# Performance work log

Measured on AMD Instinct MI355X. Metric: run time of the kernel, lower is better.

## Reference

```python
import jax, jax.numpy as jnp
import numpy as np

D_MODEL = 1024
H = 16
D_K = D_MODEL // H


def setup_inputs() -> dict:
    key = jax.random.key(0)
    ks = jax.random.split(key, 10)
    B, S = 2, 2048
    s = 1.0 / np.sqrt(D_MODEL)
    x = jax.random.normal(ks[0], (B, S, D_MODEL), dtype=jnp.float32)
    mask = jax.random.randint(ks[1], (B, 1, S, S), 0, 2, dtype=jnp.int32)
    w_q = jax.random.normal(ks[2], (D_MODEL, D_MODEL), dtype=jnp.float32) * s
    b_q = jnp.zeros((D_MODEL,), dtype=jnp.float32)
    w_k = jax.random.normal(ks[3], (D_MODEL, D_MODEL), dtype=jnp.float32) * s
    b_k = jnp.zeros((D_MODEL,), dtype=jnp.float32)
    w_v = jax.random.normal(ks[4], (D_MODEL, D_MODEL), dtype=jnp.float32) * s
    b_v = jnp.zeros((D_MODEL,), dtype=jnp.float32)
    w_o = jax.random.normal(ks[5], (D_MODEL, D_MODEL), dtype=jnp.float32) * s
    b_o = jnp.zeros((D_MODEL,), dtype=jnp.float32)
    return {"x": x, "mask": mask, "w_q": w_q, "b_q": b_q, "w_k": w_k,
            "b_k": b_k, "w_v": w_v, "b_v": b_v, "w_o": w_o, "b_o": b_o}


def reference(x, mask, w_q, b_q, w_k, b_k, w_v, b_v, w_o, b_o):
    B, S, _ = x.shape
    # projections; weights stored as (in, out) equivalents of torch Linear
    q = (x @ w_q + b_q).reshape(B, S, H, D_K).transpose(0, 2, 1, 3)  # bhsd
    k = (x @ w_k + b_k).reshape(B, S, H, D_K).transpose(0, 2, 1, 3)
    v = (x @ w_v + b_v).reshape(B, S, H, D_K).transpose(0, 2, 1, 3)
    scores = jnp.einsum('bhqd,bhkd->bhqk', q, k) / jnp.sqrt(jnp.float32(D_K))
    scores = jnp.where(mask == 0, jnp.float32(-1e9), scores)
    attn = jax.nn.softmax(scores, axis=-1)  # dropout omitted (eval mode)
    out = jnp.einsum('bhqk,bhkd->bhqd', attn, v)
    out = out.transpose(0, 2, 1, 3).reshape(B, S, D_MODEL)
    return out @ w_o + b_o
```

## Files before the change

### kernel.cpp

```cpp
#include <hip/hip_runtime.h>
#include <hip/hip_bf16.h>
#include <stdint.h>

#define D_MODEL 1024
#define NH 16
#define DK 64
#define SEQ 2048
#define BATCH 2
#define NTOK (BATCH * SEQ)

typedef __bf16 bf16;
typedef float f32x4 __attribute__((ext_vector_type(4)));
typedef __bf16 bf16x8 __attribute__((ext_vector_type(8)));
typedef __bf16 bf16x4 __attribute__((ext_vector_type(4)));
typedef __bf16 bf16x2 __attribute__((ext_vector_type(2)));

#define QSCALE 0.18033687932432668f

__device__ __forceinline__ void gload_lds16(const void* g, void* l) {
  __builtin_amdgcn_global_load_lds(
      (const __attribute__((address_space(1))) void*)g,
      (__attribute__((address_space(3))) void*)l, 16, 0, 0);
}

__global__ void prep_kernel(const float* __restrict__ x, bf16* __restrict__ xb,
                            const float* __restrict__ wq, const float* __restrict__ wk,
                            const float* __restrict__ wv, const float* __restrict__ wo,
                            bf16* __restrict__ wt,
                            const int* __restrict__ mask, unsigned long long* __restrict__ bits) {
  __shared__ float tile[32][33];
  const int bx = blockIdx.x;
  const int tid = threadIdx.x;
  if (bx < 4096) {
    int i = bx * 256 + tid;
    float4 v = reinterpret_cast<const float4*>(x)[i];
    bf16x4 o;
    o[0] = (bf16)v.x; o[1] = (bf16)v.y; o[2] = (bf16)v.z; o[3] = (bf16)v.w;
    reinterpret_cast<bf16x4*>(xb)[i] = o;
  } else if (bx < 8192) {
    int blk = bx - 4096;
    const int jt = blk & 127;
    const int kt = blk >> 7;
    const int tx = tid & 31, ty = tid >> 5;
    const int j0 = jt * 32;
    const int sel = j0 >> 10;
    const float* w = (sel == 0) ? wq : (sel == 1) ? wk : (sel == 2) ? wv : wo;
    const int jj0 = j0 & 1023;
#pragma unroll
    for (int i = 0; i < 4; ++i)
      tile[ty + i * 8][tx] = w[(size_t)(kt * 32 + ty + i * 8) * 1024 + jj0 + tx];
    __syncthreads();
#pragma unroll
    for (int i = 0; i < 4; ++i)
      wt[(size_t)(j0 + ty + i * 8) * 1024 + kt * 32 + tx] = (bf16)tile[tx][ty + i * 8];
  } else {
    int gt = (bx - 8192) * 256 + tid;
    int wid = gt >> 6;
    int l = gt & 63;
    int m = mask[(size_t)wid * 64 + l];
    unsigned long long b = __ballot(m != 0);
    if (l == 0) bits[wid] = b;
  }
}

__global__ __launch_bounds__(256) void gemm_qkv(
    const bf16* __restrict__ A, const bf16* __restrict__ Bt,
    const float* __restrict__ b0, const float* __restrict__ b1, const float* __restrict__ b2,
    bf16* __restrict__ out_q, bf16* __restrict__ out_k, bf16* __restrict__ out_vt) {
  __shared__ __align__(16) bf16 As[2][128 * 32];
  __shared__ __align__(16) bf16 Bs[2][128 * 32];
  const int tid = threadIdx.x;
  const int w = tid >> 6, l = tid & 63;
  const int wr = w >> 1, wc = w & 1;
  int lin = blockIdx.x + 24 * blockIdx.y;
  int nl = (lin & 7) * 96 + (lin >> 3);
  const int m0 = (nl / 24) * 128, n0 = (nl % 24) * 128;
  f32x4 acc[4][4] = {};
  const int lrow = l >> 2;
  const int lc8 = (l & 3) * 8;

  auto STAGE = [&](int buf, int k0) {
    char* AsB = (char*)As[buf];
    char* BsB = (char*)Bs[buf];
#pragma unroll
    for (int is = 0; is < 2; ++is) {
      int arow = m0 + is * 64 + w * 16 + lrow;
      gload_lds16(A + (size_t)arow * 1024 + k0 + lc8, AsB + is * 4096 + w * 1024);
      int brow = n0 + is * 64 + w * 16 + lrow;
      gload_lds16(Bt + (size_t)brow * 1024 + k0 + lc8, BsB + is * 4096 + w * 1024);
    }
  };

  STAGE(0, 0);
  for (int it = 0; it < 32; ++it) {
    const int cur = it & 1;
    if (it < 31) {
      STAGE(cur ^ 1, (it + 1) * 32);
      __builtin_amdgcn_sched_barrier(0);
      asm volatile("s_waitcnt vmcnt(4)" ::: "memory");
    } else {
      __builtin_amdgcn_sched_barrier(0);
      asm volatile("s_waitcnt vmcnt(0)" ::: "memory");
    }
    __builtin_amdgcn_s_barrier();
    __builtin_amdgcn_sched_barrier(0);
    const bf16* Asc = As[cur];
    const bf16* Bsc = Bs[cur];
    bf16x8 af[4], bfr[4];
#pragma unroll
    for (int m = 0; m < 4; ++m)
      af[m] = *reinterpret_cast<const bf16x8*>(Asc + (wr * 64 + m * 16 + (l & 15)) * 32 + (l >> 4) * 8);
#pragma unroll
    for (int n = 0; n < 4; ++n)
      bfr[n] = *reinterpret_cast<const bf16x8*>(Bsc + (wc * 64 + n * 16 + (l & 15)) * 32 + (l >> 4) * 8);
#pragma unroll
    for (int m = 0; m < 4; ++m)
#pragma unroll
      for (int n = 0; n < 4; ++n)
        acc[m][n] = __builtin_amdgcn_mfma_f32_16x16x32_bf16(af[m], bfr[n], acc[m][n], 0, 0, 0);
    __builtin_amdgcn_sched_barrier(0);
    __builtin_amdgcn_s_barrier();
  }

#pragma unroll
  for (int m = 0; m < 4; ++m) {
    int ib = m0 + wr * 64 + m * 16 + 4 * (l >> 4);
#pragma unroll
    for (int n = 0; n < 4; ++n) {
      int j = n0 + wc * 64 + n * 16 + (l & 15);
      int sel = j >> 10, jj = j & 1023;
      const float* bp = (sel == 0) ? b0 : (sel == 1) ? b1 : b2;
      float bias = bp[jj];
      if (sel == 0) {
#pragma unroll
        for (int r = 0; r < 4; ++r)
          out_q[(size_t)(ib + r) * 1024 + jj] = (bf16)((acc[m][n][r] + bias) * QSCALE);
      } else if (sel == 1) {
#pragma unroll
        for (int r = 0; r < 4; ++r)
          out_k[(size_t)(ib + r) * 1024 + jj] = (bf16)(acc[m][n][r] + bias);
      } else {
        int hh = jj >> 6, dd = jj & 63;
        int bb = ib >> 11, ss = ib & 2047;
        bf16x4 v;
#pragma unroll
        for (int r = 0; r < 4; ++r) v[r] = (bf16)(acc[m][n][r] + bias);
        *reinterpret_cast<bf16x4*>(out_vt + ((size_t)(bb * NH + hh) * DK + dd) * SEQ + ss) = v;
      }
    }
  }
}

__global__ __launch_bounds__(256) void gemm_out(
    const bf16* __restrict__ A, const bf16* __restrict__ Bt,
    const float* __restrict__ bias, float* __restrict__ out) {
  __shared__ __align__(16) bf16 As[2][128 * 32];
  __shared__ __align__(16) bf16 Bs[2][64 * 32];
  const int tid = threadIdx.x;
  const int w = tid >> 6, l = tid & 63;
  const int wr = w >> 1, wc = w & 1;
  int lin = blockIdx.x + 16 * blockIdx.y;
  int nl = (lin & 7) * 64 + (lin >> 3);
  const int m0 = (nl >> 4) * 128, n0 = (nl & 15) * 64;
  f32x4 acc[4][2] = {};
  const int lrow = l >> 2;
  const int lc8 = (l & 3) * 8;

  auto STAGE = [&](int buf, int k0) {
    char* AsB = (char*)As[buf];
    char* BsB = (char*)Bs[buf];
#pragma unroll
    for (int is = 0; is < 2; ++is) {
      int arow = m0 + is * 64 + w * 16 + lrow;
      gload_lds16(A + (size_t)arow * 1024 + k0 + lc8, AsB + is * 4096 + w * 1024);
    }
    gload_lds16(Bt + (size_t)(n0 + w * 16 + lrow) * 1024 + k0 + lc8, BsB + w * 1024);
  };

  STAGE(0, 0);
  for (int it = 0; it < 32; ++it) {
    const int cur = it & 1;
    if (it < 31) {
      STAGE(cur ^ 1, (it + 1) * 32);
      __builtin_amdgcn_sched_barrier(0);
      asm volatile("s_waitcnt vmcnt(3)" ::: "memory");
    } else {
      __builtin_amdgcn_sched_barrier(0);
      asm volatile("s_waitcnt vmcnt(0)" ::: "memory");
    }
    __builtin_amdgcn_s_barrier();
    __builtin_amdgcn_sched_barrier(0);
    const bf16* Asc = As[cur];
    const bf16* Bsc = Bs[cur];
    bf16x8 af[4], bfr[2];
#pragma unroll
    for (int m = 0; m < 4; ++m)
      af[m] = *reinterpret_cast<const bf16x8*>(Asc + (wr * 64 + m * 16 + (l & 15)) * 32 + (l >> 4) * 8);
#pragma unroll
    for (int n = 0; n < 2; ++n)
      bfr[n] = *reinterpret_cast<const bf16x8*>(Bsc + (wc * 32 + n * 16 + (l & 15)) * 32 + (l >> 4) * 8);
#pragma unroll
    for (int m = 0; m < 4; ++m)
#pragma unroll
      for (int n = 0; n < 2; ++n)
        acc[m][n] = __builtin_amdgcn_mfma_f32_16x16x32_bf16(af[m], bfr[n], acc[m][n], 0, 0, 0);
    __builtin_amdgcn_sched_barrier(0);
    __builtin_amdgcn_s_barrier();
  }

#pragma unroll
  for (int m = 0; m < 4; ++m) {
    int ib = m0 + wr * 64 + m * 16 + 4 * (l >> 4);
#pragma unroll
    for (int n = 0; n < 2; ++n) {
      int j = n0 + wc * 32 + n * 16 + (l & 15);
      float bv = bias[j];
#pragma unroll
      for (int r = 0; r < 4; ++r)
        out[(size_t)(ib + r) * 1024 + j] = acc[m][n][r] + bv;
    }
  }
}

__global__ __launch_bounds__(256, 4) void attn_kernel(
    const bf16* __restrict__ qb, const bf16* __restrict__ kb,
    const bf16* __restrict__ vt, const unsigned long long* __restrict__ mbits,
    bf16* __restrict__ ob) {
  __shared__ __align__(16) bf16 Kbuf[2][64 * 64];
  __shared__ __align__(16) bf16 Vbuf[2][64 * 64];
  __shared__ __align__(16) bf16 Ps[4][16 * 64];
  const int tid = threadIdx.x;
  const int w = tid >> 6, l = tid & 63;
  int lin = blockIdx.x + 32 * blockIdx.y + 512 * blockIdx.z;
  int nl = (lin & 7) * 128 + (lin >> 3);
  const int qt = nl & 31, h = (nl >> 5) & 15, b = nl >> 9;
  const int q0 = qt * 64;
  const int qrow = q0 + w * 16;
  const int tok0 = b * SEQ + qrow;
  const int a = l >> 4, c = l & 15;

  bf16x8 qf[2];
#pragma unroll
  for (int kk = 0; kk < 2; ++kk)
    qf[kk] = *reinterpret_cast<const bf16x8*>(
        qb + (size_t)(tok0 + c) * 1024 + h * 64 + kk * 32 + a * 8);

  float lsum = 0.f;
  f32x4 oacc[4] = {};

  const int swz = ((l & 7) ^ (l >> 3)) * 8;
  const bf16* ksrc = kb + (size_t)(b * SEQ) * 1024 + h * 64;
  const bf16* vsrc = vt + (size_t)(b * NH + h) * DK * SEQ;
  const unsigned long long* mrow = mbits + ((size_t)(b * SEQ + qrow + c) << 5);

  auto STAGE = [&](int buf, int kt) {
    char* KsB = (char*)Kbuf[buf];
    char* VsB = (char*)Vbuf[buf];
#pragma unroll
    for (int i = 0; i < 2; ++i) {
      int row = i * 32 + w * 8 + (l >> 3);
      gload_lds16(ksrc + (size_t)(kt * 64 + row) * 1024 + swz, KsB + i * 4096 + w * 1024);
      gload_lds16(vsrc + (size_t)row * SEQ + kt * 64 + swz, VsB + i * 4096 + w * 1024);
    }
  };

  STAGE(0, 0);
  for (int kt = 0; kt < 32; ++kt) {
    const int cur = kt & 1;
    unsigned long long mw = mrow[kt];
    __builtin_amdgcn_sched_barrier(0);
    if (kt < 31) {
      STAGE(cur ^ 1, kt + 1);
      __builtin_amdgcn_sched_barrier(0);
      asm volatile("s_waitcnt vmcnt(8)" ::: "memory");
    } else {
      __builtin_amdgcn_sched_barrier(0);
      asm volatile("s_waitcnt vmcnt(0)" ::: "memory");
    }
    __builtin_amdgcn_s_barrier();
    __builtin_amdgcn_sched_barrier(0);

    const bf16* Ks = Kbuf[cur];
    const bf16* Vs = Vbuf[cur];

    f32x4 sa[4] = {};
#pragma unroll
    for (int kk = 0; kk < 2; ++kk) {
      bf16x8 kf[4];
      int cc = kk * 4 + a;
#pragma unroll
      for (int n = 0; n < 4; ++n) {
        int rr = n * 16 + c;
        kf[n] = *reinterpret_cast<const bf16x8*>(Ks + rr * 64 + ((cc ^ (rr & 7)) << 3));
      }
#pragma unroll
      for (int n = 0; n < 4; ++n)
        sa[n] = __builtin_amdgcn_mfma_f32_16x16x32_bf16(kf[n], qf[kk], sa[n], 0, 0, 0);
    }

    unsigned long long base = mw >> (a * 4);
    float ps[4][4];
#pragma unroll
    for (int n = 0; n < 4; ++n)
#pragma unroll
      for (int r = 0; r < 4; ++r) {
        bool on = (base >> (16 * n + r)) & 1ull;
        float p = on ? __builtin_amdgcn_exp2f(sa[n][r]) : 0.f;
        ps[n][r] = p;
        lsum += p;
      }
#pragma unroll
    for (int n = 0; n < 4; ++n)
#pragma unroll
      for (int pp = 0; pp < 2; ++pp) {
        int chunk = (2 * n + (a >> 1)) ^ (c & 7);
        bf16x2 v2 = {(bf16)ps[n][2 * pp], (bf16)ps[n][2 * pp + 1]};
        *reinterpret_cast<bf16x2*>(Ps[w] + c * 64 + chunk * 8 + 4 * (a & 1) + 2 * pp) = v2;
      }

#pragma unroll
    for (int kk = 0; kk < 2; ++kk) {
      bf16x8 pa = *reinterpret_cast<const bf16x8*>(Ps[w] + c * 64 + (((a + 4 * kk) ^ (c & 7)) << 3));
      bf16x8 vf[4];
#pragma unroll
      for (int dn = 0; dn < 4; ++dn) {
        int rr = dn * 16 + c;
        vf[dn] = *reinterpret_cast<const bf16x8*>(Vs + rr * 64 + (((kk * 4 + a) ^ (rr & 7)) << 3));
      }
#pragma unroll
      for (int dn = 0; dn < 4; ++dn)
        oacc[dn] = __builtin_amdgcn_mfma_f32_16x16x32_bf16(pa, vf[dn], oacc[dn], 0, 0, 0);
    }
    __builtin_amdgcn_sched_barrier(0);
    __builtin_amdgcn_s_barrier();
  }

  float s = lsum;
  s += __shfl_xor(s, 16);
  s += __shfl_xor(s, 32);
#pragma unroll
  for (int r = 0; r < 4; ++r) {
    float sr = __shfl(s, 4 * a + r);
    float inv = 1.f / fmaxf(sr, 1e-35f);
    int tok = tok0 + 4 * a + r;
#pragma unroll
    for (int dn = 0; dn < 4; ++dn)
      ob[(size_t)tok * 1024 + h * 64 + dn * 16 + c] = (bf16)(oacc[dn][r] * inv);
  }
}

extern "C" void kernel_launch(void* const* d_in, const int* in_sizes, int n_in,
                              void* d_out, int out_size, void* d_ws, size_t ws_size,
                              hipStream_t stream) {
  const float* x = (const float*)d_in[0];
  const int* mask = (const int*)d_in[1];
  const float* wq = (const float*)d_in[2];
  const float* bq = (const float*)d_in[3];
  const float* wk = (const float*)d_in[4];
  const float* bk = (const float*)d_in[5];
  const float* wv = (const float*)d_in[6];
  const float* bv = (const float*)d_in[7];
  const float* wo = (const float*)d_in[8];
  const float* bo = (const float*)d_in[9];
  float* out = (float*)d_out;

  char* ws = (char*)d_ws;
  bf16* xb = (bf16*)(ws + (size_t)0);
  bf16* wt = (bf16*)(ws + ((size_t)8 << 20));
  bf16* qb = (bf16*)(ws + ((size_t)16 << 20));
  bf16* kb = (bf16*)(ws + ((size_t)24 << 20));
  bf16* vtb = (bf16*)(ws + ((size_t)32 << 20));
  bf16* ob = (bf16*)(ws + ((size_t)40 << 20));
  unsigned long long* mbits = (unsigned long long*)(ws + ((size_t)48 << 20));

  prep_kernel<<<40960, 256, 0, stream>>>(x, xb, wq, wk, wv, wo, wt, mask, mbits);
  gemm_qkv<<<dim3(24, 32), 256, 0, stream>>>(xb, wt, bq, bk, bv, qb, kb, vtb);
  attn_kernel<<<dim3(32, NH, BATCH), 256, 0, stream>>>(qb, kb, vtb, mbits, ob);
  gemm_out<<<dim3(16, 32), 256, 0, stream>>>(ob, wt + (size_t)3072 * 1024, bo, out);
}
```

Measured before the change: 234.4 us.

## Use single-buffered BK=64 swizzled GEMM tiles, XCD-aware block mapping, tweak attention waits

Both projection GEMMs drop the double-buffered BK=32 pipeline and use a single LDS buffer with BK=64 and an XOR-swizzled layout, with plain __syncthreads between the load and compute phases. Block-to-tile mapping is reworked so each XCD owns a contiguous band of N columns, which is meant to improve L2 reuse of the weights. In attention, the vmcnt wait count changes from 8 to 5 and the P-tile stores widen from bf16x2 to bf16x4. Giving up double buffering exposes global load latency in exchange for fewer barriers and conflict-free LDS reads. The vmcnt(5) value looks inconsistent with 4 outstanding loads per stage and may over-wait or under-wait.

Result: no change. 238.5 us (+1.8%).

```diff
diff --git a/kernel.cpp b/kernel.cpp
--- a/kernel.cpp
+++ b/kernel.cpp
@@ -13,7 +13,6 @@
 typedef float f32x4 __attribute__((ext_vector_type(4)));
 typedef __bf16 bf16x8 __attribute__((ext_vector_type(8)));
 typedef __bf16 bf16x4 __attribute__((ext_vector_type(4)));
-typedef __bf16 bf16x2 __attribute__((ext_vector_type(2)));
 
 #define QSCALE 0.18033687932432668f
 
@@ -67,59 +66,45 @@
     const bf16* __restrict__ A, const bf16* __restrict__ Bt,
     const float* __restrict__ b0, const float* __restrict__ b1, const float* __restrict__ b2,
     bf16* __restrict__ out_q, bf16* __restrict__ out_k, bf16* __restrict__ out_vt) {
-  __shared__ __align__(16) bf16 As[2][128 * 32];
-  __shared__ __align__(16) bf16 Bs[2][128 * 32];
+  __shared__ __align__(16) bf16 As[128 * 64];
+  __shared__ __align__(16) bf16 Bs[128 * 64];
   const int tid = threadIdx.x;
   const int w = tid >> 6, l = tid & 63;
   const int wr = w >> 1, wc = w & 1;
   int lin = blockIdx.x + 24 * blockIdx.y;
-  int nl = (lin & 7) * 96 + (lin >> 3);
-  const int m0 = (nl / 24) * 128, n0 = (nl % 24) * 128;
+  int xcd = lin & 7, idx = lin >> 3;
+  const int n0 = (xcd * 3 + idx % 3) * 128;
+  const int m0 = (idx / 3) * 128;
   f32x4 acc[4][4] = {};
-  const int lrow = l >> 2;
-  const int lc8 = (l & 3) * 8;
-
-  auto STAGE = [&](int buf, int k0) {
-    char* AsB = (char*)As[buf];
-    char* BsB = (char*)Bs[buf];
-#pragma unroll
-    for (int is = 0; is < 2; ++is) {
-      int arow = m0 + is * 64 + w * 16 + lrow;
-      gload_lds16(A + (size_t)arow * 1024 + k0 + lc8, AsB + is * 4096 + w * 1024);
-      int brow = n0 + is * 64 + w * 16 + lrow;
-      gload_lds16(Bt + (size_t)brow * 1024 + k0 + lc8, BsB + is * 4096 + w * 1024);
-    }
-  };
-
-  STAGE(0, 0);
-  for (int it = 0; it < 32; ++it) {
-    const int cur = it & 1;
-    if (it < 31) {
-      STAGE(cur ^ 1, (it + 1) * 32);
-      __builtin_amdgcn_sched_barrier(0);
-      asm volatile("s_waitcnt vmcnt(4)" ::: "memory");
-    } else {
-      __builtin_amdgcn_sched_barrier(0);
-      asm volatile("s_waitcnt vmcnt(0)" ::: "memory");
-    }
-    __builtin_amdgcn_s_barrier();
-    __builtin_amdgcn_sched_barrier(0);
-    const bf16* Asc = As[cur];
-    const bf16* Bsc = Bs[cur];
-    bf16x8 af[4], bfr[4];
-#pragma unroll
-    for (int m = 0; m < 4; ++m)
-      af[m] = *reinterpret_cast<const bf16x8*>(Asc + (wr * 64 + m * 16 + (l & 15)) * 32 + (l >> 4) * 8);
-#pragma unroll
-    for (int n = 0; n < 4; ++n)
-      bfr[n] = *reinterpret_cast<const bf16x8*>(Bsc + (wc * 64 + n * 16 + (l & 15)) * 32 + (l >> 4) * 8);
-#pragma unroll
-    for (int m = 0; m < 4; ++m)
+  const int srow = w * 8 + (l >> 3);
+  const int ssw = ((l & 7) ^ (l >> 3)) * 8;
+  char* AsB = (char*)As;
+  char* BsB = (char*)Bs;
+
+  for (int k0 = 0; k0 < 1024; k0 += 64) {
+#pragma unroll
+    for (int i = 0; i < 4; ++i) {
+      gload_lds16(A + (size_t)(m0 + i * 32 + srow) * 1024 + k0 + ssw, AsB + i * 4096 + w * 1024);
+      gload_lds16(Bt + (size_t)(n0 + i * 32 + srow) * 1024 + k0 + ssw, BsB + i * 4096 + w * 1024);
+    }
+    __syncthreads();
+#pragma unroll
+    for (int kk = 0; kk < 2; ++kk) {
+      const int cc = (((kk * 4 + (l >> 4)) ^ (l & 7)) << 3);
+      bf16x8 af[4], bfr[4];
+#pragma unroll
+      for (int m = 0; m < 4; ++m)
+        af[m] = *reinterpret_cast<const bf16x8*>(As + (wr * 64 + m * 16 + (l & 15)) * 64 + cc);
 #pragma unroll
       for (int n = 0; n < 4; ++n)
-        acc[m][n] = __builtin_amdgcn_mfma_f32_16x16x32_bf16(af[m], bfr[n], acc[m][n], 0, 0, 0);
-    __builtin_amdgcn_sched_barrier(0);
-    __builtin_amdgcn_s_barrier();
+        bfr[n] = *reinterpret_cast<const bf16x8*>(Bs + (wc * 64 + n * 16 + (l & 15)) * 64 + cc);
+#pragma unroll
+      for (int m = 0; m < 4; ++m)
+#pragma unroll
+        for (int n = 0; n < 4; ++n)
+          acc[m][n] = __builtin_amdgcn_mfma_f32_16x16x32_bf16(af[m], bfr[n], acc[m][n], 0, 0, 0);
+    }
+    __syncthreads();
   }
 
 #pragma unroll
@@ -154,58 +139,46 @@
 __global__ __launch_bounds__(256) void gemm_out(
     const bf16* __restrict__ A, const bf16* __restrict__ Bt,
     const float* __restrict__ bias, float* __restrict__ out) {
-  __shared__ __align__(16) bf16 As[2][128 * 32];
-  __shared__ __align__(16) bf16 Bs[2][64 * 32];
+  __shared__ __align__(16) bf16 As[128 * 64];
+  __shared__ __align__(16) bf16 Bs[64 * 64];
   const int tid = threadIdx.x;
   const int w = tid >> 6, l = tid & 63;
   const int wr = w >> 1, wc = w & 1;
   int lin = blockIdx.x + 16 * blockIdx.y;
-  int nl = (lin & 7) * 64 + (lin >> 3);
-  const int m0 = (nl >> 4) * 128, n0 = (nl & 15) * 64;
+  int xcd = lin & 7, idx = lin >> 3;
+  const int n0 = (xcd * 2 + idx % 2) * 64;
+  const int m0 = (idx / 2) * 128;
   f32x4 acc[4][2] = {};
-  const int lrow = l >> 2;
-  const int lc8 = (l & 3) * 8;
-
-  auto STAGE = [&](int buf, int k0) {
-    char* AsB = (char*)As[buf];
-    char* BsB = (char*)Bs[buf];
-#pragma unroll
-    for (int is = 0; is < 2; ++is) {
-      int arow = m0 + is * 64 + w * 16 + lrow;
-      gload_lds16(A + (size_t)arow * 1024 + k0 + lc8, AsB + is * 4096 + w * 1024);
-    }
-    gload_lds16(Bt + (size_t)(n0 + w * 16 + lrow) * 1024 + k0 + lc8, BsB + w * 1024);
-  };
-
-  STAGE(0, 0);
-  for (int it = 0; it < 32; ++it) {
-    const int cur = it & 1;
-    if (it < 31) {
-      STAGE(cur ^ 1, (it + 1) * 32);
-      __builtin_amdgcn_sched_barrier(0);
-      asm volatile("s_waitcnt vmcnt(3)" ::: "memory");
-    } else {
-      __builtin_amdgcn_sched_barrier(0);
-      asm volatile("s_waitcnt vmcnt(0)" ::: "memory");
-    }
-    __builtin_amdgcn_s_barrier();
-    __builtin_amdgcn_sched_barrier(0);
-    const bf16* Asc = As[cur];
-    const bf16* Bsc = Bs[cur];
-    bf16x8 af[4], bfr[2];
-#pragma unroll
-    for (int m = 0; m < 4; ++m)
-      af[m] = *reinterpret_cast<const bf16x8*>(Asc + (wr * 64 + m * 16 + (l & 15)) * 32 + (l >> 4) * 8);
-#pragma unroll
-    for (int n = 0; n < 2; ++n)
-      bfr[n] = *reinterpret_cast<const bf16x8*>(Bsc + (wc * 32 + n * 16 + (l & 15)) * 32 + (l >> 4) * 8);
-#pragma unroll
-    for (int m = 0; m < 4; ++m)
+  const int srow = w * 8 + (l >> 3);
+  const int ssw = ((l & 7) ^ (l >> 3)) * 8;
+  char* AsB = (char*)As;
+  char* BsB = (char*)Bs;
+
+  for (int k0 = 0; k0 < 1024; k0 += 64) {
+#pragma unroll
+    for (int i = 0; i < 4; ++i)
+      gload_lds16(A + (size_t)(m0 + i * 32 + srow) * 1024 + k0 + ssw, AsB + i * 4096 + w * 1024);
+#pragma unroll
+    for (int i = 0; i < 2; ++i)
+      gload_lds16(Bt + (size_t)(n0 + i * 32 + srow) * 1024 + k0 + ssw, BsB + i * 4096 + w * 1024);
+    __syncthreads();
+#pragma unroll
+    for (int kk = 0; kk < 2; ++kk) {
+      const int cc = (((kk * 4 + (l >> 4)) ^ (l & 7)) << 3);
+      bf16x8 af[4], bfr[2];
+#pragma unroll
+      for (int m = 0; m < 4; ++m)
+        af[m] = *reinterpret_cast<const bf16x8*>(As + (wr * 64 + m * 16 + (l & 15)) * 64 + cc);
 #pragma unroll
       for (int n = 0; n < 2; ++n)
-        acc[m][n] = __builtin_amdgcn_mfma_f32_16x16x32_bf16(af[m], bfr[n], acc[m][n], 0, 0, 0);
-    __builtin_amdgcn_sched_barrier(0);
-    __builtin_amdgcn_s_barrier();
+        bfr[n] = *reinterpret_cast<const bf16x8*>(Bs + (wc * 32 + n * 16 + (l & 15)) * 64 + cc);
+#pragma unroll
+      for (int m = 0; m < 4; ++m)
+#pragma unroll
+        for (int n = 0; n < 2; ++n)
+          acc[m][n] = __builtin_amdgcn_mfma_f32_16x16x32_bf16(af[m], bfr[n], acc[m][n], 0, 0, 0);
+    }
+    __syncthreads();
   }
 
 #pragma unroll
@@ -272,7 +245,7 @@
     if (kt < 31) {
       STAGE(cur ^ 1, kt + 1);
       __builtin_amdgcn_sched_barrier(0);
-      asm volatile("s_waitcnt vmcnt(8)" ::: "memory");
+      asm volatile("s_waitcnt vmcnt(5)" ::: "memory");
     } else {
       __builtin_amdgcn_sched_barrier(0);
       asm volatile("s_waitcnt vmcnt(0)" ::: "memory");
@@ -310,13 +283,13 @@
         lsum += p;
       }
 #pragma unroll
-    for (int n = 0; n < 4; ++n)
-#pragma unroll
-      for (int pp = 0; pp < 2; ++pp) {
-        int chunk = (2 * n + (a >> 1)) ^ (c & 7);
-        bf16x2 v2 = {(bf16)ps[n][2 * pp], (bf16)ps[n][2 * pp + 1]};
-        *reinterpret_cast<bf16x2*>(Ps[w] + c * 64 + chunk * 8 + 4 * (a & 1) + 2 * pp) = v2;
-      }
+    for (int n = 0; n < 4; ++n) {
+      int chunk = (2 * n + (a >> 1)) ^ (c & 7);
+      bf16x4 v4;
+      v4[0] = (bf16)ps[n][0]; v4[1] = (bf16)ps[n][1];
+      v4[2] = (bf16)ps[n][2]; v4[3] = (bf16)ps[n][3];
+      *reinterpret_cast<bf16x4*>(Ps[w] + c * 64 + chunk * 8 + 4 * (a & 1)) = v4;
+    }
 
 #pragma unroll
     for (int kk = 0; kk < 2; ++kk) {
```
